# Kernel optimization log

Hardware: AMD Instinct MI355X
Metric: run time of the kernel (lower is better)

The kernel has to match this reference:

```python
import jax, jax.numpy as jnp
import numpy as np

D_MODEL = 1024
N_HEAD = 16
D_HEAD = D_MODEL // N_HEAD
EXP = 4
B, T = 2, 2048
EPS = 1e-5

def setup_inputs() -> dict:
    key = jax.random.key(0)
    ks = jax.random.split(key, 16)
    s = 0.02
    return {
        "x": jax.random.normal(ks[0], (B, T, D_MODEL), jnp.float32),
        "ln1_w": jnp.ones((D_MODEL,), jnp.float32),
        "ln1_b": jnp.zeros((D_MODEL,), jnp.float32),
        "attn_w": jax.random.normal(ks[1], (D_MODEL, 3 * D_MODEL), jnp.float32) * s,
        "attn_b": jnp.zeros((3 * D_MODEL,), jnp.float32),
        "proj_w": jax.random.normal(ks[2], (D_MODEL, D_MODEL), jnp.float32) * s,
        "proj_b": jnp.zeros((D_MODEL,), jnp.float32),
        "ln2_w": jnp.ones((D_MODEL,), jnp.float32),
        "ln2_b": jnp.zeros((D_MODEL,), jnp.float32),
        "fc_w": jax.random.normal(ks[3], (D_MODEL, EXP * D_MODEL), jnp.float32) * s,
        "fc_b": jnp.zeros((EXP * D_MODEL,), jnp.float32),
        "fc2_w": jax.random.normal(ks[4], (EXP * D_MODEL, D_MODEL), jnp.float32) * s,
        "fc2_b": jnp.zeros((D_MODEL,), jnp.float32),
    }

def _layernorm(x, w, b):
    mu = jnp.mean(x, axis=-1, keepdims=True)
    var = jnp.mean(jnp.square(x - mu), axis=-1, keepdims=True)
    return (x - mu) * jax.lax.rsqrt(var + EPS) * w + b

def _attn(x, attn_w, attn_b, proj_w, proj_b):
    Bx, Tx, C = x.shape
    qkv = x @ attn_w + attn_b  # [B,T,3C]
    q, k, v = jnp.split(qkv, 3, axis=-1)
    # [B, H, T, Dh]
    q = q.reshape(Bx, Tx, N_HEAD, D_HEAD).transpose(0, 2, 1, 3)
    k = k.reshape(Bx, Tx, N_HEAD, D_HEAD).transpose(0, 2, 1, 3)
    v = v.reshape(Bx, Tx, N_HEAD, D_HEAD).transpose(0, 2, 1, 3)
    att = jnp.einsum('bhqd,bhkd->bhqk', q, k) * (1.0 / np.sqrt(D_HEAD))
    causal = jnp.tril(jnp.ones((Tx, Tx), bool))
    att = jnp.where(causal, att, -jnp.inf)
    att = jax.nn.softmax(att, axis=-1)
    y = jnp.einsum('bhqk,bhkd->bhqd', att, v)
    y = y.transpose(0, 2, 1, 3).reshape(Bx, Tx, C)
    return y @ proj_w + proj_b

def reference(x, ln1_w, ln1_b, attn_w, attn_b, proj_w, proj_b,
              ln2_w, ln2_b, fc_w, fc_b, fc2_w, fc2_b):
    x = x + _attn(_layernorm(x, ln1_w, ln1_b), attn_w, attn_b, proj_w, proj_b)
    h = _layernorm(x, ln2_w, ln2_b)
    h = jax.nn.gelu(h @ fc_w + fc_b, approximate=False)  # exact GELU (torch nn.GELU default)
    x = x + (h @ fc2_w + fc2_b)
    return x
```

## Files before the change

### kernel.cpp

```cpp
#include <hip/hip_runtime.h>
#include <hip/hip_bf16.h>
#include <math.h>


#define D_MODEL 1024
#define N_HEAD  16
#define D_HEAD  64
#define SEQ_T   2048
#define BATCH   2
#define NROWS   (BATCH * SEQ_T)
#define C3      (3 * D_MODEL)
#define D_FF    (4 * D_MODEL)

typedef __bf16 bf16x8 __attribute__((ext_vector_type(8)));
typedef __bf16 bf16x4t __attribute__((ext_vector_type(4)));
typedef short  s16x4  __attribute__((ext_vector_type(4)));
typedef float  f32x4  __attribute__((ext_vector_type(4)));

#define WAIT_VM8() asm volatile("s_waitcnt vmcnt(8)" ::: "memory")

__device__ __forceinline__ f32x4 mfma16_bf16(s16x4 a, s16x4 b, f32x4 c)
{
#if __has_builtin(__builtin_amdgcn_mfma_f32_16x16x16_bf16)
    return __builtin_amdgcn_mfma_f32_16x16x16_bf16(
        __builtin_bit_cast(bf16x4t, a), __builtin_bit_cast(bf16x4t, b), c, 0, 0, 0);
#else
    return __builtin_amdgcn_mfma_f32_16x16x16bf16_1k(a, b, c, 0, 0, 0);
#endif
}

__global__ __launch_bounds__(256) void ln_kernel(
    const float* __restrict__ in, const float* __restrict__ w,
    const float* __restrict__ b, __hip_bfloat16* __restrict__ out, int D)
{
    const int row = blockIdx.x;
    const int tid = threadIdx.x;
    const float* x = in + (size_t)row * D;

    float s = 0.f, s2 = 0.f;
    for (int i = tid; i < D; i += 256) {
        float v = x[i];
        s += v; s2 += v * v;
    }
    __shared__ float rs[256], rs2[256];
    rs[tid] = s; rs2[tid] = s2;
    __syncthreads();
    for (int off = 128; off > 0; off >>= 1) {
        if (tid < off) { rs[tid] += rs[tid + off]; rs2[tid] += rs2[tid + off]; }
        __syncthreads();
    }
    const float mu   = rs[0] / D;
    const float var  = rs2[0] / D - mu * mu;
    const float rstd = rsqrtf(var + 1e-5f);

    __hip_bfloat16* o = out + (size_t)row * D;
    for (int i = tid; i < D; i += 256)
        o[i] = __float2bfloat16((x[i] - mu) * rstd * w[i] + b[i]);
}

__global__ __launch_bounds__(256) void transpose_all_kernel(
    const float* __restrict__ attn_w, const float* __restrict__ proj_w,
    const float* __restrict__ fc_w,   const float* __restrict__ fc2_w,
    __hip_bfloat16* __restrict__ attn_wt, __hip_bfloat16* __restrict__ proj_wt,
    __hip_bfloat16* __restrict__ fc_wt,   __hip_bfloat16* __restrict__ fc2_wt)
{
    __shared__ float t[32][33];
    int tb = blockIdx.x;
    const float* W; __hip_bfloat16* Wt; int K, N;
    if (tb < 3072)      { W = attn_w; Wt = attn_wt; K = D_MODEL; N = C3; }
    else if (tb < 4096) { tb -= 3072; W = proj_w; Wt = proj_wt; K = D_MODEL; N = D_MODEL; }
    else if (tb < 8192) { tb -= 4096; W = fc_w;   Wt = fc_wt;   K = D_MODEL; N = D_FF; }
    else                { tb -= 8192; W = fc2_w;  Wt = fc2_wt;  K = D_FF;    N = D_MODEL; }
    const int ntx = N >> 5;
    const int k0 = (tb / ntx) * 32;
    const int n0 = (tb % ntx) * 32;

    const int tx = threadIdx.x & 31;
    const int ty = threadIdx.x >> 5;
#pragma unroll
    for (int i = 0; i < 4; ++i)
        t[ty + 8 * i][tx] = W[(size_t)(k0 + ty + 8 * i) * N + n0 + tx];
    __syncthreads();
#pragma unroll
    for (int i = 0; i < 4; ++i)
        Wt[(size_t)(n0 + ty + 8 * i) * K + k0 + tx] =
            __float2bfloat16(t[tx][ty + 8 * i]);
}

__device__ __forceinline__ void async16(const __hip_bfloat16* g, __hip_bfloat16* l)
{
    __builtin_amdgcn_global_load_lds(
        (const __attribute__((address_space(1))) void*)g,
        (__attribute__((address_space(3))) void*)l, 16, 0, 0);
}

__device__ __forceinline__ float gelu_exact(float v)
{
    return 0.5f * v * (1.0f + erff(v * 0.70710678118654752f));
}

__device__ __forceinline__ void swz_xcd(int& bx, int& by)
{
    const int nbx = gridDim.x;
    const int nwg = nbx * gridDim.y;
    int lin = blockIdx.y * nbx + blockIdx.x;
    const int per = nwg >> 3;
    lin = (lin & 7) * per + (lin >> 3);
    bx = lin % nbx;
    by = lin / nbx;
}


template<int NL, int TPB>
__device__ __forceinline__ void stage_slice(
    const __hip_bfloat16* __restrict__ g, int K,
    __hip_bfloat16* __restrict__ ldst, int tid)
{
#pragma unroll
    for (int i = 0; i < NL; ++i)
        async16(g + (size_t)(i * (TPB / 4)) * K, ldst + i * (TPB / 4) * 32 + tid * 8);
}

__device__ __forceinline__ void gemm_rot4_512(
    const __hip_bfloat16* __restrict__ A,
    const __hip_bfloat16* __restrict__ Bt,
    int K, int row0, int col0, f32x4 (&acc)[8][4])
{
    __shared__ __align__(16) __hip_bfloat16 Asl[4][256 * 32];
    __shared__ __align__(16) __hip_bfloat16 Bsl[4][256 * 32];

    const int tid  = threadIdx.x;
    const int wv   = tid >> 6;
    const int lane = tid & 63;
    const int ln15 = lane & 15;
    const int lq   = lane >> 4;
    const int mbase = (wv >> 2) * 128;
    const int nbase = (wv & 3) * 64;
    const int rcol = (lq ^ ((ln15 >> 1) & 3)) * 8;
    const int ssw  = ((tid & 3) ^ ((tid >> 3) & 3)) * 8;
    const __hip_bfloat16* Ab = A  + (size_t)(row0 + (tid >> 2)) * K + ssw;
    const __hip_bfloat16* Bb = Bt + (size_t)(col0 + (tid >> 2)) * K + ssw;
    const int nt = K >> 5;

#pragma unroll
    for (int mi = 0; mi < 8; ++mi)
#pragma unroll
        for (int ni = 0; ni < 4; ++ni) acc[mi][ni] = (f32x4){0.f, 0.f, 0.f, 0.f};

#pragma unroll
    for (int t = 0; t < 3; ++t) {
        stage_slice<2, 512>(Ab + t * 32, K, &Asl[t][0], tid);
        stage_slice<2, 512>(Bb + t * 32, K, &Bsl[t][0], tid);
    }
    WAIT_VM8();
    __builtin_amdgcn_s_barrier();

    for (int tq = 0; tq < nt; tq += 4) {
#pragma unroll
        for (int u = 0; u < 4; ++u) {
            const int t   = tq + u;
            const int tcl = (t + 3 < nt) ? t + 3 : nt - 1;
            const int sl  = u;
            const int sl3 = (u + 3) & 3;
            bf16x8 af[4], bfr[4];

#pragma unroll
            for (int mi = 0; mi < 4; ++mi)
                af[mi] = *(const bf16x8*)&Asl[sl][(mbase + mi * 16 + ln15) * 32 + rcol];
#pragma unroll
            for (int ni = 0; ni < 4; ++ni)
                bfr[ni] = *(const bf16x8*)&Bsl[sl][(nbase + ni * 16 + ln15) * 32 + rcol];
            stage_slice<2, 512>(Ab + (size_t)tcl * 32, K, &Asl[sl3][0], tid);
            __builtin_amdgcn_s_barrier();
            __builtin_amdgcn_s_setprio(1);
#pragma unroll
            for (int mi = 0; mi < 4; ++mi)
#pragma unroll
                for (int ni = 0; ni < 4; ++ni)
                    acc[mi][ni] = __builtin_amdgcn_mfma_f32_16x16x32_bf16(
                        af[mi], bfr[ni], acc[mi][ni], 0, 0, 0);
            __builtin_amdgcn_s_setprio(0);
            __builtin_amdgcn_s_barrier();

#pragma unroll
            for (int mi = 0; mi < 4; ++mi)
                af[mi] = *(const bf16x8*)&Asl[sl][(mbase + 64 + mi * 16 + ln15) * 32 + rcol];
            stage_slice<2, 512>(Bb + (size_t)tcl * 32, K, &Bsl[sl3][0], tid);
            WAIT_VM8();
            __builtin_amdgcn_s_barrier();
            __builtin_amdgcn_s_setprio(1);
#pragma unroll
            for (int mi = 0; mi < 4; ++mi)
#pragma unroll
                for (int ni = 0; ni < 4; ++ni)
                    acc[4 + mi][ni] = __builtin_amdgcn_mfma_f32_16x16x32_bf16(
                        af[mi], bfr[ni], acc[4 + mi][ni], 0, 0, 0);
            __builtin_amdgcn_s_setprio(0);
            __builtin_amdgcn_s_barrier();
        }
    }
}

__device__ __forceinline__ void gemm_rot4_256(
    const __hip_bfloat16* __restrict__ A,
    const __hip_bfloat16* __restrict__ Bt,
    int K, int row0, int col0, f32x4 (&acc)[4][4])
{
    __shared__ __align__(16) __hip_bfloat16 Asl[4][128 * 32];
    __shared__ __align__(16) __hip_bfloat16 Bsl[4][128 * 32];

    const int tid  = threadIdx.x;
    const int wv   = tid >> 6;
    const int lane = tid & 63;
    const int ln15 = lane & 15;
    const int lq   = lane >> 4;
    const int mbase = (wv >> 1) * 64;
    const int nbase = (wv & 1) * 64;
    const int rcol = (lq ^ ((ln15 >> 1) & 3)) * 8;
    const int ssw  = ((tid & 3) ^ ((tid >> 3) & 3)) * 8;
    const __hip_bfloat16* Ab = A  + (size_t)(row0 + (tid >> 2)) * K + ssw;
    const __hip_bfloat16* Bb = Bt + (size_t)(col0 + (tid >> 2)) * K + ssw;
    const int nt = K >> 5;

#pragma unroll
    for (int mi = 0; mi < 4; ++mi)
#pragma unroll
        for (int ni = 0; ni < 4; ++ni) acc[mi][ni] = (f32x4){0.f, 0.f, 0.f, 0.f};

#pragma unroll
    for (int t = 0; t < 3; ++t) {
        stage_slice<2, 256>(Ab + t * 32, K, &Asl[t][0], tid);
        stage_slice<2, 256>(Bb + t * 32, K, &Bsl[t][0], tid);
    }
    WAIT_VM8();
    __builtin_amdgcn_s_barrier();

    for (int tq = 0; tq < nt; tq += 4) {
#pragma unroll
        for (int u = 0; u < 4; ++u) {
            const int t   = tq + u;
            const int tcl = (t + 3 < nt) ? t + 3 : nt - 1;
            const int sl  = u;
            const int sl3 = (u + 3) & 3;
            bf16x8 af[4], bfr[4];

#pragma unroll
            for (int mi = 0; mi < 4; ++mi)
                af[mi] = *(const bf16x8*)&Asl[sl][(mbase + mi * 16 + ln15) * 32 + rcol];
#pragma unroll
            for (int ni = 0; ni < 4; ++ni)
                bfr[ni] = *(const bf16x8*)&Bsl[sl][(nbase + ni * 16 + ln15) * 32 + rcol];
            stage_slice<2, 256>(Ab + (size_t)tcl * 32, K, &Asl[sl3][0], tid);
            stage_slice<2, 256>(Bb + (size_t)tcl * 32, K, &Bsl[sl3][0], tid);
            WAIT_VM8();
            __builtin_amdgcn_s_barrier();
            __builtin_amdgcn_s_setprio(1);
#pragma unroll
            for (int mi = 0; mi < 4; ++mi)
#pragma unroll
                for (int ni = 0; ni < 4; ++ni)
                    acc[mi][ni] = __builtin_amdgcn_mfma_f32_16x16x32_bf16(
                        af[mi], bfr[ni], acc[mi][ni], 0, 0, 0);
            __builtin_amdgcn_s_setprio(0);
            __builtin_amdgcn_s_barrier();
        }
    }
}

__global__ __launch_bounds__(512) void gemm256_kernel(
    const __hip_bfloat16* __restrict__ A,
    const __hip_bfloat16* __restrict__ Bt,
    const float* __restrict__ bias,
    const float* __restrict__ residual,
    void* __restrict__ Cout,
    int M, int N, int K, int act, int outBf16)
{
    int bx, by;
    swz_xcd(bx, by);
    const int row0 = by * 256;
    const int col0 = bx * 256;

    f32x4 acc[8][4];
    gemm_rot4_512(A, Bt, K, row0, col0, acc);

    const int tid  = threadIdx.x;
    const int wv   = tid >> 6;
    const int lane = tid & 63;
    const int ln15 = lane & 15;
    const int lq   = lane >> 4;
    const int mbase = (wv >> 2) * 128;
    const int nbase = (wv & 3) * 64;

#pragma unroll
    for (int mi = 0; mi < 8; ++mi) {
#pragma unroll
        for (int ni = 0; ni < 4; ++ni) {
            const int gc = col0 + nbase + ni * 16 + ln15;
            const float bv = bias[gc];
#pragma unroll
            for (int r = 0; r < 4; ++r) {
                const int gr = row0 + mbase + mi * 16 + lq * 4 + r;
                float v = acc[mi][ni][r] + bv;
                if (act == 1) v = gelu_exact(v);
                if (residual) v += residual[(size_t)gr * N + gc];
                if (outBf16)
                    ((__hip_bfloat16*)Cout)[(size_t)gr * N + gc] = __float2bfloat16(v);
                else
                    ((float*)Cout)[(size_t)gr * N + gc] = v;
            }
        }
    }
}

__global__ __launch_bounds__(256, 2) void gemm128_kernel(
    const __hip_bfloat16* __restrict__ A,
    const __hip_bfloat16* __restrict__ Bt,
    const float* __restrict__ bias,
    const float* __restrict__ residual,
    void* __restrict__ Cout,
    int M, int N, int K, int act, int outBf16)
{
    int bx, by;
    swz_xcd(bx, by);
    const int row0 = by * 128;
    const int col0 = bx * 128;

    f32x4 acc[4][4];
    gemm_rot4_256(A, Bt, K, row0, col0, acc);

    const int tid  = threadIdx.x;
    const int wv   = tid >> 6;
    const int lane = tid & 63;
    const int ln15 = lane & 15;
    const int lq   = lane >> 4;
    const int mbase = (wv >> 1) * 64;
    const int nbase = (wv & 1) * 64;

#pragma unroll
    for (int mi = 0; mi < 4; ++mi) {
#pragma unroll
        for (int ni = 0; ni < 4; ++ni) {
            const int gc = col0 + nbase + ni * 16 + ln15;
            const float bv = bias[gc];
#pragma unroll
            for (int r = 0; r < 4; ++r) {
                const int gr = row0 + mbase + mi * 16 + lq * 4 + r;
                float v = acc[mi][ni][r] + bv;
                if (act == 1) v = gelu_exact(v);
                if (residual) v += residual[(size_t)gr * N + gc];
                if (outBf16)
                    ((__hip_bfloat16*)Cout)[(size_t)gr * N + gc] = __float2bfloat16(v);
                else
                    ((float*)Cout)[(size_t)gr * N + gc] = v;
            }
        }
    }
}

__global__ __launch_bounds__(512) void qkv256_kernel(
    const __hip_bfloat16* __restrict__ A,
    const __hip_bfloat16* __restrict__ Bt,
    const float* __restrict__ bias,
    __hip_bfloat16* __restrict__ Qb,
    __hip_bfloat16* __restrict__ Kb,
    __hip_bfloat16* __restrict__ Vtb)
{
    int bx, by;
    swz_xcd(bx, by);
    const int row0 = by * 256;
    const int col0 = bx * 256;

    f32x4 acc[8][4];
    gemm_rot4_512(A, Bt, D_MODEL, row0, col0, acc);

    const int tid  = threadIdx.x;
    const int wv   = tid >> 6;
    const int lane = tid & 63;
    const int ln15 = lane & 15;
    const int lq   = lane >> 4;
    const int mbase = (wv >> 2) * 128;
    const int nbase = (wv & 3) * 64;

#pragma unroll
    for (int mi = 0; mi < 8; ++mi) {
        const int gr0 = row0 + mbase + mi * 16 + lq * 4;
        const int bb  = gr0 >> 11;
        const int q0  = gr0 & 2047;
#pragma unroll
        for (int ni = 0; ni < 4; ++ni) {
            const int gc  = col0 + nbase + ni * 16 + ln15;
            const float bv = bias[gc];
            const int sec = gc >> 10;
            const int hd  = (gc & 1023) >> 6;
            const int d   = gc & 63;
            if (sec == 2) {
                unsigned short u[4];
#pragma unroll
                for (int r = 0; r < 4; ++r) {
                    __hip_bfloat16 e = __float2bfloat16(acc[mi][ni][r] + bv);
                    u[r] = *(unsigned short*)&e;
                }
                uint2 pk;
                pk.x = (unsigned int)u[0] | ((unsigned int)u[1] << 16);
                pk.y = (unsigned int)u[2] | ((unsigned int)u[3] << 16);
                *(uint2*)(Vtb + ((size_t)((bb * N_HEAD + hd) * D_HEAD + d)) * SEQ_T + q0) = pk;
            } else {
                __hip_bfloat16* dst = (sec == 0 ? Qb : Kb)
                    + ((size_t)((bb * N_HEAD + hd) * SEQ_T + q0)) * D_HEAD + d;
#pragma unroll
                for (int r = 0; r < 4; ++r)
                    dst[(size_t)r * D_HEAD] = __float2bfloat16(acc[mi][ni][r] + bv);
            }
        }
    }
}

#define ATQ 64
#define ATK 128
#define NQT (SEQ_T / ATQ)

__global__ __launch_bounds__(256) void mfma_attn_kernel(
    const __hip_bfloat16* __restrict__ Qb,
    const __hip_bfloat16* __restrict__ Kb,
    const __hip_bfloat16* __restrict__ Vtb,
    __hip_bfloat16* __restrict__ y)
{
    __shared__ __align__(16) __hip_bfloat16 Ks[ATK * D_HEAD];
    __shared__ __align__(16) __hip_bfloat16 Vts[D_HEAD * ATK];

    const int flat = (blockIdx.z * gridDim.y + blockIdx.y) * gridDim.x + blockIdx.x;
    const int xcd  = flat & 7;
    const int slot = flat >> 3;
    const int pair = slot & 15;
    const int hb   = slot >> 4;
    const int h    = xcd + 8 * (hb & 1);
    const int b    = hb >> 1;

    const int tid  = threadIdx.x;
    const int wv   = tid >> 6;
    const int lane = tid & 63;
    const int ln15 = lane & 15;
    const int lq   = lane >> 4;

    const __hip_bfloat16* Qh = Qb  + (size_t)(b * N_HEAD + h) * SEQ_T * D_HEAD;
    const __hip_bfloat16* Kh = Kb  + (size_t)(b * N_HEAD + h) * SEQ_T * D_HEAD;
    const __hip_bfloat16* Vh = Vtb + (size_t)(b * N_HEAD + h) * D_HEAD * SEQ_T;
    const size_t bT = (size_t)b * SEQ_T;

    const float CEXP = 0.18033688011f;

    bf16x8 kreg[4], vreg[4];
    const int kr = tid >> 3, kg = tid & 7;
    const int vr = tid >> 4, vc = tid & 15;

    auto issue = [&](int kb) {
#pragma unroll
        for (int i = 0; i < 4; ++i)
            kreg[i] = *(const bf16x8*)(Kh + (size_t)(kb + kr + i * 32) * D_HEAD + kg * 8);
#pragma unroll
        for (int i = 0; i < 4; ++i)
            vreg[i] = *(const bf16x8*)(Vh + (size_t)(vr + i * 16) * SEQ_T + kb + vc * 8);
    };
    auto commit = [&]() {
#pragma unroll
        for (int i = 0; i < 4; ++i) {
            const int r = kr + i * 32;
            *(bf16x8*)&Ks[r * 64 + ((kg ^ (r & 7)) << 3)] = kreg[i];
        }
#pragma unroll
        for (int i = 0; i < 4; ++i) {
            const int r = vr + i * 16;
            const int g8 = vc * 2;
            *(bf16x8*)&Vts[r * 128 + ((g8 ^ ((r & 3) << 2)) << 2)] = vreg[i];
        }
    };

#pragma unroll 1
    for (int half = 0; half < 2; ++half) {
        const int qt    = half == 0 ? pair : (NQT - 1 - pair);
        const int qbase = qt * ATQ;
        const int ntk   = (qt >> 1) + 1;
        const int qg    = qbase + wv * 16 + ln15;

        bf16x8 qf[2];
#pragma unroll
        for (int kc = 0; kc < 2; ++kc)
            qf[kc] = *(const bf16x8*)(Qh + (size_t)(qbase + wv * 16 + ln15) * D_HEAD
                                      + kc * 32 + lq * 8);

        f32x4 Oacc[4];
#pragma unroll
        for (int dn = 0; dn < 4; ++dn) Oacc[dn] = (f32x4){0.f, 0.f, 0.f, 0.f};
        float m_run = -INFINITY, l_run = 0.f;

        issue(0);

        for (int t = 0; t < ntk; ++t) {
            const int kb = t * ATK;
            commit();
            __syncthreads();
            if (t + 1 < ntk) issue((t + 1) * ATK);

            f32x4 st[8];
#pragma unroll
            for (int jf = 0; jf < 8; ++jf) st[jf] = (f32x4){0.f, 0.f, 0.f, 0.f};
            __builtin_amdgcn_s_setprio(1);
#pragma unroll
            for (int jf = 0; jf < 8; ++jf) {
                const int rw = jf * 16 + ln15;
                const bf16x8 kf0 = *(const bf16x8*)&Ks[rw * 64 + ((lq ^ (ln15 & 7)) << 3)];
                const bf16x8 kf1 = *(const bf16x8*)&Ks[rw * 64 + (((4 + lq) ^ (ln15 & 7)) << 3)];
                st[jf] = __builtin_amdgcn_mfma_f32_16x16x32_bf16(kf0, qf[0], st[jf], 0, 0, 0);
                st[jf] = __builtin_amdgcn_mfma_f32_16x16x32_bf16(kf1, qf[1], st[jf], 0, 0, 0);
            }
            __builtin_amdgcn_s_setprio(0);

            if (t == ntk - 1) {
#pragma unroll
                for (int jf = 0; jf < 8; ++jf)
#pragma unroll
                    for (int r = 0; r < 4; ++r)
                        if ((kb + jf * 16 + lq * 4 + r) > qg) st[jf][r] = -INFINITY;
            }

            float tmax = st[0][0];
#pragma unroll
            for (int jf = 0; jf < 8; ++jf)
#pragma unroll
                for (int r = 0; r < 4; ++r) tmax = fmaxf(tmax, st[jf][r]);
            tmax = fmaxf(tmax, __shfl_xor(tmax, 16));
            tmax = fmaxf(tmax, __shfl_xor(tmax, 32));
            const float mnew  = fmaxf(m_run, tmax);
            const float alpha = exp2f((m_run - mnew) * CEXP);
            const float mc    = mnew * CEXP;
            float psum = 0.f;
#pragma unroll
            for (int jf = 0; jf < 8; ++jf)
#pragma unroll
                for (int r = 0; r < 4; ++r) {
                    const float p = exp2f(fmaf(st[jf][r], CEXP, -mc));
                    st[jf][r] = p;
                    psum += p;
                }
            psum += __shfl_xor(psum, 16);
            psum += __shfl_xor(psum, 32);
            l_run = alpha * l_run + psum;
            m_run = mnew;

            float a4[4];
#pragma unroll
            for (int r = 0; r < 4; ++r) a4[r] = __shfl(alpha, lq * 4 + r);
#pragma unroll
            for (int dn = 0; dn < 4; ++dn)
#pragma unroll
                for (int r = 0; r < 4; ++r) Oacc[dn][r] *= a4[r];

            __builtin_amdgcn_s_setprio(1);
#pragma unroll
            for (int jf = 0; jf < 8; ++jf) {
                s16x4 pfr;
#pragma unroll
                for (int s = 0; s < 4; ++s) {
                    __hip_bfloat16 e = __float2bfloat16(st[jf][s]);
                    pfr[s] = __builtin_bit_cast(short, e);
                }
#pragma unroll
                for (int dn = 0; dn < 4; ++dn) {
                    const int rw = dn * 16 + ln15;
                    const int g8 = (jf * 4 + lq) ^ ((ln15 & 3) << 2);
                    const s16x4 vfr = *(const s16x4*)&Vts[rw * 128 + (g8 << 2)];
                    Oacc[dn] = mfma16_bf16(pfr, vfr, Oacc[dn]);
                }
            }
            __builtin_amdgcn_s_setprio(0);
            __syncthreads();
        }

        float il[4];
#pragma unroll
        for (int r = 0; r < 4; ++r) il[r] = 1.0f / __shfl(l_run, lq * 4 + r);
#pragma unroll
        for (int dn = 0; dn < 4; ++dn)
#pragma unroll
            for (int r = 0; r < 4; ++r)
                Ks[(wv * 16 + lq * 4 + r) * 72 + dn * 16 + ln15] =
                    __float2bfloat16(Oacc[dn][r] * il[r]);
        const int r2 = lane >> 3, c8 = (lane & 7) * 8;
#pragma unroll
        for (int i = 0; i < 2; ++i) {
            const int row = wv * 16 + r2 + 8 * i;
            const bf16x8 val = *(const bf16x8*)&Ks[row * 72 + c8];
            *(bf16x8*)(y + (bT + qbase + row) * D_MODEL + h * D_HEAD + c8) = val;
        }
        __syncthreads();
    }
}

extern "C" void kernel_launch(void* const* d_in, const int* in_sizes, int n_in,
                              void* d_out, int out_size, void* d_ws, size_t ws_size,
                              hipStream_t stream)
{
    const float* x      = (const float*)d_in[0];
    const float* ln1_w  = (const float*)d_in[1];
    const float* ln1_b  = (const float*)d_in[2];
    const float* attn_w = (const float*)d_in[3];
    const float* attn_b = (const float*)d_in[4];
    const float* proj_w = (const float*)d_in[5];
    const float* proj_b = (const float*)d_in[6];
    const float* ln2_w  = (const float*)d_in[7];
    const float* ln2_b  = (const float*)d_in[8];
    const float* fc_w   = (const float*)d_in[9];
    const float* fc_b   = (const float*)d_in[10];
    const float* fc2_w  = (const float*)d_in[11];
    const float* fc2_b  = (const float*)d_in[12];
    float* out = (float*)d_out;

    char* ws = (char*)d_ws;
    __hip_bfloat16* Qb      = (__hip_bfloat16*)(ws);
    __hip_bfloat16* Kb      = (__hip_bfloat16*)(ws + (size_t)8  * 1024 * 1024);
    __hip_bfloat16* Vtb     = (__hip_bfloat16*)(ws + (size_t)16 * 1024 * 1024);
    __hip_bfloat16* h_bf    = (__hip_bfloat16*)(ws);
    __hip_bfloat16* ln_buf  = (__hip_bfloat16*)(ws + (size_t)32 * 1024 * 1024);
    __hip_bfloat16* y_buf   = (__hip_bfloat16*)(ws + (size_t)40 * 1024 * 1024);
    float*          xmid    = (float*)(ws + (size_t)48 * 1024 * 1024);
    __hip_bfloat16* attn_wt = (__hip_bfloat16*)(ws + (size_t)64 * 1024 * 1024);
    __hip_bfloat16* proj_wt = (__hip_bfloat16*)(ws + (size_t)70 * 1024 * 1024);
    __hip_bfloat16* fc_wt   = (__hip_bfloat16*)(ws + (size_t)72 * 1024 * 1024);
    __hip_bfloat16* fc2_wt  = (__hip_bfloat16*)(ws + (size_t)80 * 1024 * 1024);

    dim3 blk256(256);
    dim3 blk512(512);

    transpose_all_kernel<<<dim3(12288), blk256, 0, stream>>>(
        attn_w, proj_w, fc_w, fc2_w, attn_wt, proj_wt, fc_wt, fc2_wt);

    ln_kernel<<<dim3(NROWS), blk256, 0, stream>>>(x, ln1_w, ln1_b, ln_buf, D_MODEL);

    qkv256_kernel<<<dim3(C3 / 256, NROWS / 256), blk512, 0, stream>>>(
        ln_buf, attn_wt, attn_b, Qb, Kb, Vtb);

    mfma_attn_kernel<<<dim3(NQT / 2, N_HEAD, BATCH), blk256, 0, stream>>>(
        Qb, Kb, Vtb, y_buf);

    gemm128_kernel<<<dim3(D_MODEL / 128, NROWS / 128), blk256, 0, stream>>>(
        y_buf, proj_wt, proj_b, x, xmid, NROWS, D_MODEL, D_MODEL, 0, 0);

    ln_kernel<<<dim3(NROWS), blk256, 0, stream>>>(xmid, ln2_w, ln2_b, ln_buf, D_MODEL);

    gemm256_kernel<<<dim3(D_FF / 256, NROWS / 256), blk512, 0, stream>>>(
        ln_buf, fc_wt, fc_b, nullptr, h_bf, NROWS, D_FF, D_MODEL, 1, 1);

    gemm128_kernel<<<dim3(D_MODEL / 128, NROWS / 128), blk256, 0, stream>>>(
        h_bf, fc2_wt, fc2_b, xmid, out, NROWS, D_MODEL, D_FF, 0, 0);
}
```

Before: 388.6 us.

## Use 8-wave 128x128 GEMM tiles and re-layout attention K/V shared memory

The 128x128 GEMM used for the proj and fc2 layers now runs with 512 threads (8 waves), each computing a 32x64 sub-tile instead of 64x64. Staging is spread over more threads and the wait count is lowered to match. The goal is more waves in flight to hide latency on these N=1024 GEMMs, at the cost of fewer MFMAs per wave and more LDS fragment reloads per FLOP. Separately, the attention kernel splits K into two 32-column halves with an XOR swizzle and stores V^T with padded rows (stride 136) instead of XOR swizzling, aiming to cut bank conflicts and index arithmetic.

```diff
diff --git a/kernel.cpp b/kernel.cpp
--- a/kernel.cpp
+++ b/kernel.cpp
@@ -18,6 +18,7 @@
 typedef float  f32x4  __attribute__((ext_vector_type(4)));
 
 #define WAIT_VM8() asm volatile("s_waitcnt vmcnt(8)" ::: "memory")
+#define WAIT_VM4() asm volatile("s_waitcnt vmcnt(4)" ::: "memory")
 
 __device__ __forceinline__ f32x4 mfma16_bf16(s16x4 a, s16x4 b, f32x4 c)
 {
@@ -201,10 +202,10 @@
     }
 }
 
-__device__ __forceinline__ void gemm_rot4_256(
+__device__ __forceinline__ void gemm_rot4_128x8(
     const __hip_bfloat16* __restrict__ A,
     const __hip_bfloat16* __restrict__ Bt,
-    int K, int row0, int col0, f32x4 (&acc)[4][4])
+    int K, int row0, int col0, f32x4 (&acc)[2][4])
 {
     __shared__ __align__(16) __hip_bfloat16 Asl[4][128 * 32];
     __shared__ __align__(16) __hip_bfloat16 Bsl[4][128 * 32];
@@ -214,7 +215,7 @@
     const int lane = tid & 63;
     const int ln15 = lane & 15;
     const int lq   = lane >> 4;
-    const int mbase = (wv >> 1) * 64;
+    const int mbase = (wv >> 1) * 32;
     const int nbase = (wv & 1) * 64;
     const int rcol = (lq ^ ((ln15 >> 1) & 3)) * 8;
     const int ssw  = ((tid & 3) ^ ((tid >> 3) & 3)) * 8;
@@ -223,16 +224,16 @@
     const int nt = K >> 5;
 
 #pragma unroll
-    for (int mi = 0; mi < 4; ++mi)
+    for (int mi = 0; mi < 2; ++mi)
 #pragma unroll
         for (int ni = 0; ni < 4; ++ni) acc[mi][ni] = (f32x4){0.f, 0.f, 0.f, 0.f};
 
 #pragma unroll
     for (int t = 0; t < 3; ++t) {
-        stage_slice<2, 256>(Ab + t * 32, K, &Asl[t][0], tid);
-        stage_slice<2, 256>(Bb + t * 32, K, &Bsl[t][0], tid);
-    }
-    WAIT_VM8();
+        stage_slice<1, 512>(Ab + t * 32, K, &Asl[t][0], tid);
+        stage_slice<1, 512>(Bb + t * 32, K, &Bsl[t][0], tid);
+    }
+    WAIT_VM4();
     __builtin_amdgcn_s_barrier();
 
     for (int tq = 0; tq < nt; tq += 4) {
@@ -242,21 +243,21 @@
             const int tcl = (t + 3 < nt) ? t + 3 : nt - 1;
             const int sl  = u;
             const int sl3 = (u + 3) & 3;
-            bf16x8 af[4], bfr[4];
-
-#pragma unroll
-            for (int mi = 0; mi < 4; ++mi)
+            bf16x8 af[2], bfr[4];
+
+#pragma unroll
+            for (int mi = 0; mi < 2; ++mi)
                 af[mi] = *(const bf16x8*)&Asl[sl][(mbase + mi * 16 + ln15) * 32 + rcol];
 #pragma unroll
             for (int ni = 0; ni < 4; ++ni)
                 bfr[ni] = *(const bf16x8*)&Bsl[sl][(nbase + ni * 16 + ln15) * 32 + rcol];
-            stage_slice<2, 256>(Ab + (size_t)tcl * 32, K, &Asl[sl3][0], tid);
-            stage_slice<2, 256>(Bb + (size_t)tcl * 32, K, &Bsl[sl3][0], tid);
-            WAIT_VM8();
+            stage_slice<1, 512>(Ab + (size_t)tcl * 32, K, &Asl[sl3][0], tid);
+            stage_slice<1, 512>(Bb + (size_t)tcl * 32, K, &Bsl[sl3][0], tid);
+            WAIT_VM4();
             __builtin_amdgcn_s_barrier();
             __builtin_amdgcn_s_setprio(1);
 #pragma unroll
-            for (int mi = 0; mi < 4; ++mi)
+            for (int mi = 0; mi < 2; ++mi)
 #pragma unroll
                 for (int ni = 0; ni < 4; ++ni)
                     acc[mi][ni] = __builtin_amdgcn_mfma_f32_16x16x32_bf16(
@@ -312,7 +313,7 @@
     }
 }
 
-__global__ __launch_bounds__(256, 2) void gemm128_kernel(
+__global__ __launch_bounds__(512, 2) void gemm128_kernel(
     const __hip_bfloat16* __restrict__ A,
     const __hip_bfloat16* __restrict__ Bt,
     const float* __restrict__ bias,
@@ -325,19 +326,19 @@
     const int row0 = by * 128;
     const int col0 = bx * 128;
 
-    f32x4 acc[4][4];
-    gemm_rot4_256(A, Bt, K, row0, col0, acc);
+    f32x4 acc[2][4];
+    gemm_rot4_128x8(A, Bt, K, row0, col0, acc);
 
     const int tid  = threadIdx.x;
     const int wv   = tid >> 6;
     const int lane = tid & 63;
     const int ln15 = lane & 15;
     const int lq   = lane >> 4;
-    const int mbase = (wv >> 1) * 64;
+    const int mbase = (wv >> 1) * 32;
     const int nbase = (wv & 1) * 64;
 
 #pragma unroll
-    for (int mi = 0; mi < 4; ++mi) {
+    for (int mi = 0; mi < 2; ++mi) {
 #pragma unroll
         for (int ni = 0; ni < 4; ++ni) {
             const int gc = col0 + nbase + ni * 16 + ln15;
@@ -418,6 +419,7 @@
 #define ATQ 64
 #define ATK 128
 #define NQT (SEQ_T / ATQ)
+#define VP2 136
 
 __global__ __launch_bounds__(256) void mfma_attn_kernel(
     const __hip_bfloat16* __restrict__ Qb,
@@ -425,8 +427,8 @@
     const __hip_bfloat16* __restrict__ Vtb,
     __hip_bfloat16* __restrict__ y)
 {
-    __shared__ __align__(16) __hip_bfloat16 Ks[ATK * D_HEAD];
-    __shared__ __align__(16) __hip_bfloat16 Vts[D_HEAD * ATK];
+    __shared__ __align__(16) __hip_bfloat16 Ks[2 * ATK * 32];
+    __shared__ __align__(16) __hip_bfloat16 Vts[D_HEAD * VP2];
 
     const int flat = (blockIdx.z * gridDim.y + blockIdx.y) * gridDim.x + blockIdx.x;
     const int xcd  = flat & 7;
@@ -452,6 +454,8 @@
     bf16x8 kreg[4], vreg[4];
     const int kr = tid >> 3, kg = tid & 7;
     const int vr = tid >> 4, vc = tid & 15;
+    const int khalf = kg >> 2;
+    const int kpos  = (kg & 3) ^ ((kr >> 1) & 3);
 
     auto issue = [&](int kb) {
 #pragma unroll
@@ -465,15 +469,16 @@
 #pragma unroll
         for (int i = 0; i < 4; ++i) {
             const int r = kr + i * 32;
-            *(bf16x8*)&Ks[r * 64 + ((kg ^ (r & 7)) << 3)] = kreg[i];
+            *(bf16x8*)&Ks[khalf * (ATK * 32) + r * 32 + kpos * 8] = kreg[i];
         }
 #pragma unroll
         for (int i = 0; i < 4; ++i) {
             const int r = vr + i * 16;
-            const int g8 = vc * 2;
-            *(bf16x8*)&Vts[r * 128 + ((g8 ^ ((r & 3) << 2)) << 2)] = vreg[i];
+            *(bf16x8*)&Vts[r * VP2 + vc * 8] = vreg[i];
         }
     };
+
+    const int rcol = (lq ^ ((ln15 >> 1) & 3)) * 8;
 
 #pragma unroll 1
     for (int half = 0; half < 2; ++half) {
@@ -508,8 +513,8 @@
 #pragma unroll
             for (int jf = 0; jf < 8; ++jf) {
                 const int rw = jf * 16 + ln15;
-                const bf16x8 kf0 = *(const bf16x8*)&Ks[rw * 64 + ((lq ^ (ln15 & 7)) << 3)];
-                const bf16x8 kf1 = *(const bf16x8*)&Ks[rw * 64 + (((4 + lq) ^ (ln15 & 7)) << 3)];
+                const bf16x8 kf0 = *(const bf16x8*)&Ks[rw * 32 + rcol];
+                const bf16x8 kf1 = *(const bf16x8*)&Ks[ATK * 32 + rw * 32 + rcol];
                 st[jf] = __builtin_amdgcn_mfma_f32_16x16x32_bf16(kf0, qf[0], st[jf], 0, 0, 0);
                 st[jf] = __builtin_amdgcn_mfma_f32_16x16x32_bf16(kf1, qf[1], st[jf], 0, 0, 0);
             }
@@ -566,9 +571,8 @@
                 }
 #pragma unroll
                 for (int dn = 0; dn < 4; ++dn) {
-                    const int rw = dn * 16 + ln15;
-                    const int g8 = (jf * 4 + lq) ^ ((ln15 & 3) << 2);
-                    const s16x4 vfr = *(const s16x4*)&Vts[rw * 128 + (g8 << 2)];
+                    const s16x4 vfr = *(const s16x4*)&Vts[(dn * 16 + ln15) * VP2
+                                                          + jf * 16 + lq * 4];
                     Oacc[dn] = mfma16_bf16(pfr, vfr, Oacc[dn]);
                 }
             }
@@ -642,7 +646,7 @@
     mfma_attn_kernel<<<dim3(NQT / 2, N_HEAD, BATCH), blk256, 0, stream>>>(
         Qb, Kb, Vtb, y_buf);
 
-    gemm128_kernel<<<dim3(D_MODEL / 128, NROWS / 128), blk256, 0, stream>>>(
+    gemm128_kernel<<<dim3(D_MODEL / 128, NROWS / 128), blk512, 0, stream>>>(
         y_buf, proj_wt, proj_b, x, xmid, NROWS, D_MODEL, D_MODEL, 0, 0);
 
     ln_kernel<<<dim3(NROWS), blk256, 0, stream>>>(xmid, ln2_w, ln2_b, ln_buf, D_MODEL);
@@ -650,6 +654,6 @@
     gemm256_kernel<<<dim3(D_FF / 256, NROWS / 256), blk512, 0, stream>>>(
         ln_buf, fc_wt, fc_b, nullptr, h_bf, NROWS, D_FF, D_MODEL, 1, 1);
 
-    gemm128_kernel<<<dim3(D_MODEL / 128, NROWS / 128), blk256, 0, stream>>>(
+    gemm128_kernel<<<dim3(D_MODEL / 128, NROWS / 128), blk512, 0, stream>>>(
         h_bf, fc2_wt, fc2_b, xmid, out, NROWS, D_MODEL, D_FF, 0, 0);
 }
```

Measured after the change: 360.2 us. -7.3%, faster.
